# Kernel optimization log

Hardware: AMD Instinct MI355X
Metric: run time of the kernel (lower is better)

## Reference

```python
import jax, jax.numpy as jnp
import numpy as np

EPS = 1e-5  # torch BatchNorm2d default eps

# BinaryActivation with STE: grad zeroed where |x| >= 1 (the extra 1.3 clip in
# xnor_binarize.backward is a subset and thus redundant).
@jax.custom_vjp
def sign_act(x):
    return jnp.sign(x)

def _sa_fwd(x):
    return jnp.sign(x), x

def _sa_bwd(x, g):
    mask = ((x > -1.0) & (x < 1.0)).astype(g.dtype)
    return (g * mask,)

sign_act.defvjp(_sa_fwd, _sa_bwd)

# Weight binarization (scale=False path): w.data.clamp_(-1,1) then sign();
# backward is straight-through identity (|bi_weight|=1 < 1.3 so clip never fires).
@jax.custom_vjp
def bin_weight(w):
    return jnp.sign(jnp.clip(w, -1.0, 1.0))

def _bw_fwd(w):
    return jnp.sign(jnp.clip(w, -1.0, 1.0)), None

def _bw_bwd(_, g):
    return (g,)

bin_weight.defvjp(_bw_fwd, _bw_bwd)


def _branch(x, gamma, beta, w, bias):
    # BatchNorm2d (training-mode batch stats, biased var), affine
    mu = jnp.mean(x, axis=(0, 2, 3), keepdims=True)
    var = jnp.var(x, axis=(0, 2, 3), keepdims=True)
    h = (x - mu) * jax.lax.rsqrt(var + EPS)
    h = h * gamma[None, :, None, None] + beta[None, :, None, None]
    # XNOR conv: binarized activations and weights, stride 2, pad 1
    a = sign_act(h)
    bw = bin_weight(w)
    y = jax.lax.conv_general_dilated(
        a, bw, window_strides=(2, 2), padding=[(1, 1), (1, 1)],
        dimension_numbers=('NCHW', 'OIHW', 'NCHW'))
    y = y + bias[None, :, None, None]
    # shortcut: AvgPool2d(kernel_size=2) (stride defaults to 2)
    B, C, H, W = x.shape
    sc = x.reshape(B, C, H // 2, 2, W // 2, 2).mean(axis=(3, 5))
    return jax.nn.relu(y) + sc


def setup_inputs() -> dict:
    key = jax.random.key(0)
    ks = jax.random.split(key, 9)
    B, C, H, W = 32, 192, 64, 64
    K = 3
    x = jax.random.normal(ks[0], (B, C, H, W), dtype=jnp.float32)
    g1 = 1.0 + 0.1 * jax.random.normal(ks[1], (C,), dtype=jnp.float32)
    b1 = 0.1 * jax.random.normal(ks[2], (C,), dtype=jnp.float32)
    w1 = 0.05 * jax.random.normal(ks[3], (C, C, K, K), dtype=jnp.float32)
    bias1 = jnp.zeros((C,), dtype=jnp.float32)
    g2 = 1.0 + 0.1 * jax.random.normal(ks[4], (C,), dtype=jnp.float32)
    b2 = 0.1 * jax.random.normal(ks[5], (C,), dtype=jnp.float32)
    w2 = 0.05 * jax.random.normal(ks[6], (C, C, K, K), dtype=jnp.float32)
    bias2 = jnp.zeros((C,), dtype=jnp.float32)
    return {"x": x, "g1": g1, "b1": b1, "w1": w1, "bias1": bias1,
            "g2": g2, "b2": b2, "w2": w2, "bias2": bias2}


def reference(x, g1, b1, w1, bias1, g2, b2, w2, bias2):
    x1 = _branch(x, g1, b1, w1, bias1)
    x2 = _branch(x, g2, b2, w2, bias2)
    return jnp.concatenate([x1, x2], axis=1)  # [B, 2C, H/2, W/2]
```

## Files before the change

### kernel.cpp

```cpp
#include <hip/hip_runtime.h>
#include <hip/hip_bf16.h>

typedef unsigned int u32;

#define BN 32
#define CC 192
#define HH 64
#define WW 64
#define HWSZ (HH*WW)
#define OHH 32
#define OWW 32
#define NVALID_SCALE 131072.0f
#define PLW 65
#define PLSZ (PLW*PLW)
#define NPLANE (12*BN)

__global__ __launch_bounds__(256) void k_stats(const float* __restrict__ x,
                                               float* __restrict__ partial) {
    int b = blockIdx.x;
    int c = b >> 5, n = b & 31;
    const float4* p = (const float4*)(x + ((size_t)(n * CC + c) << 12));
    int tid = threadIdx.x;
    float s = 0.f, s2 = 0.f;
#pragma unroll
    for (int k = 0; k < 4; ++k) {
        float4 f = p[tid + 256 * k];
        s  += f.x + f.y + f.z + f.w;
        s2 += f.x * f.x + f.y * f.y + f.z * f.z + f.w * f.w;
    }
#pragma unroll
    for (int off = 32; off > 0; off >>= 1) {
        s  += __shfl_down(s, off, 64);
        s2 += __shfl_down(s2, off, 64);
    }
    __shared__ float red[8];
    int wv = tid >> 6, ln = tid & 63;
    if (ln == 0) { red[wv * 2] = s; red[wv * 2 + 1] = s2; }
    __syncthreads();
    if (tid == 0) {
        partial[b * 2]     = red[0] + red[2] + red[4] + red[6];
        partial[b * 2 + 1] = red[1] + red[3] + red[5] + red[7];
    }
}

__global__ __launch_bounds__(64) void k_coef(const float* __restrict__ partial,
        const float* __restrict__ g1, const float* __restrict__ b1,
        const float* __restrict__ g2, const float* __restrict__ b2,
        float* __restrict__ coef) {
    int c = blockIdx.x;
    int t = threadIdx.x;
    int half = t >> 5, i = t & 31;
    float v = partial[(c * 32 + i) * 2 + half];
#pragma unroll
    for (int off = 16; off > 0; off >>= 1) v += __shfl_down(v, off, 32);
    float S2 = __shfl(v, 32, 64);
    if (t == 0) {
        float S = v;
        const float inv = 1.0f / NVALID_SCALE;
        float mu  = S * inv;
        float var = S2 * inv - mu * mu;
        float r   = 1.0f / sqrtf(var + 1e-5f);
        float s1 = g1[c] * r, t1 = b1[c] - mu * s1;
        float s2 = g2[c] * r, t2 = b2[c] - mu * s2;
        ((float4*)coef)[c] = make_float4(s1, t1, s2, t2);
    }
}

__global__ __launch_bounds__(256) void k_pack_w(const float* __restrict__ w1,
        const float* __restrict__ w2, u32* __restrict__ wp, u32* __restrict__ wsum) {
    __shared__ float wl[CC * 9];
    __shared__ u32 ww[54];
    int b  = blockIdx.x;
    int br = b / CC, oc = b - br * CC;
    const float* W = (br ? w2 : w1) + (size_t)oc * CC * 9;
    int tid = threadIdx.x;
    for (int i = tid; i < CC * 9; i += 256) wl[i] = W[i];
    __syncthreads();
    if (tid < 54) {
        int w6 = tid % 6, pos = tid / 6;
        u32 word = 0;
#pragma unroll
        for (int bb = 0; bb < 32; ++bb) {
            if (wl[(w6 * 32 + bb) * 9 + pos] > 0.f) word |= (1u << bb);
        }
        wp[(size_t)b * 54 + tid] = word;
        ww[tid] = word;
    }
    __syncthreads();
    if (tid == 0) {
        int Wt[9];
#pragma unroll
        for (int t = 0; t < 9; ++t) {
            int s = 0;
#pragma unroll
            for (int w6 = 0; w6 < 6; ++w6) s += __popc(ww[t * 6 + w6]);
            Wt[t] = s;
        }
        wsum[b * 4 + 0] = (u32)(Wt[0] + Wt[1] + Wt[2]);
        wsum[b * 4 + 1] = (u32)(Wt[0] + Wt[3] + Wt[6]);
        wsum[b * 4 + 2] = (u32)Wt[0];
        wsum[b * 4 + 3] = 0;
    }
}

__global__ __launch_bounds__(192) void k_halo(u32* __restrict__ act) {
    u32* pl = act + (size_t)blockIdx.x * PLSZ;
    int t = threadIdx.x;
    if (t < PLW) pl[t] = 0;
    else if (t < 2 * PLW - 1) pl[(t - PLW + 1) * PLW] = 0;
}

__global__ __launch_bounds__(256) void k_pack_act(const float* __restrict__ x,
        const float* __restrict__ coef, u32* __restrict__ act) {
    int tile = blockIdx.x;
    int g    = blockIdx.y;
    int n = tile >> 4, pxt = tile & 15;
    int px = pxt * 256 + threadIdx.x;
    int h = px >> 6, w = px & 63;
    const float*  xb = x + (size_t)n * CC * HWSZ + px;
    const float4* c4 = (const float4*)coef;
    u32 pk1 = 0, pk2 = 0;
#pragma unroll 8
    for (int bb = 0; bb < 32; ++bb) {
        int ch = g * 32 + bb;
        float v = xb[(size_t)ch * HWSZ];
        float4 cf = c4[ch];
        u32 bit = 1u << bb;
        if (v * cf.x + cf.y > 0.f) pk1 |= bit;
        if (v * cf.z + cf.w > 0.f) pk2 |= bit;
    }
    size_t off = (size_t)(h + 1) * PLW + (w + 1);
    act[((size_t)(0 * 6 + g) * BN + n) * PLSZ + off] = pk1;
    act[((size_t)(1 * 6 + g) * BN + n) * PLSZ + off] = pk2;
}

__global__ __launch_bounds__(256, 4) void k_conv(
        const u32* __restrict__ act, const u32* __restrict__ wp,
        const u32* __restrict__ wsum, const float* __restrict__ x,
        const float* __restrict__ bias1, const float* __restrict__ bias2,
        float* __restrict__ out) {
    __shared__ u32 s_act[12 * 5 * PLW];
    int b    = blockIdx.x;
    int tile = b >> 2;
    int n    = tile >> 4, ohp = tile & 15;
    int tid  = threadIdx.x;
    {
        int rowbase = 4 * ohp;
        for (int i = tid; i < 12 * 5 * PLW; i += 256) {
            int q   = i / (5 * PLW);
            int rem = i - q * (5 * PLW);
            s_act[i] = act[((size_t)q * BN + n) * PLSZ + (size_t)rowbase * PLW + rem];
        }
    }
    __syncthreads();
    int wid  = __builtin_amdgcn_readfirstlane((int)(tid >> 6));
    int ocbase = ((b & 3) * 4 + wid) * 12;
    int lane = tid & 63;
    int ow = lane & 31, lh = lane >> 5;
    int oh = 2 * ohp + lh;
    int topE  = (oh == 0), leftE = (ow == 0);
    int nv192 = CC * ((topE ? 2 : 3) * (leftE ? 2 : 3));
    int lloc = (2 * lh) * PLW + 2 * ow;
    float sc[12];
#pragma unroll 1
    for (int br = 0; br < 2; ++br) {
        u32 a[54];
#pragma unroll
        for (int w6 = 0; w6 < 6; ++w6) {
            const u32* ap = &s_act[(br * 6 + w6) * 5 * PLW + lloc];
#pragma unroll
            for (int t = 0; t < 9; ++t) {
                a[t * 6 + w6] = ap[(t / 3) * PLW + (t % 3)];
            }
        }
        const u32*   wqb = wp   + (size_t)(br * CC + ocbase) * 54;
        const u32*   wsb = wsum + (size_t)(br * CC + ocbase) * 4;
        const float* bsp = (br ? bias2 : bias1) + ocbase;
#pragma unroll 2
        for (int j = 0; j < 12; ++j) {
            u32 wv[54];
#pragma unroll
            for (int k = 0; k < 54; ++k) wv[k] = wqb[j * 54 + k];
            int p = 0;
#pragma unroll
            for (int k = 0; k < 54; ++k) p += __popc(a[k] ^ wv[k]);
            int Wr = (int)wsb[j * 4], Wc = (int)wsb[j * 4 + 1], Wk = (int)wsb[j * 4 + 2];
            int corr = (topE ? Wr : 0) + (leftE ? Wc : 0) - ((topE & leftE) ? Wk : 0);
            int dot = nv192 - 2 * p + 2 * corr;
            int oc = ocbase + j;
            float y = (float)dot + bsp[j];
            if (br == 0) {
                const float* xp = x + (((size_t)n * CC + oc) * HH + 2 * oh) * WW + 2 * ow;
                float2 r0 = *(const float2*)xp;
                float2 r1 = *(const float2*)(xp + WW);
                sc[j] = (r0.x + r0.y + r1.x + r1.y) * 0.25f;
            }
            out[((size_t)(n * 384 + br * CC + oc) * OHH + oh) * OWW + ow] =
                fmaxf(y, 0.f) + sc[j];
        }
    }
}

extern "C" void kernel_launch(void* const* d_in, const int* in_sizes, int n_in,
                              void* d_out, int out_size, void* d_ws, size_t ws_size,
                              hipStream_t stream) {
    const float* x     = (const float*)d_in[0];
    const float* g1    = (const float*)d_in[1];
    const float* b1    = (const float*)d_in[2];
    const float* w1    = (const float*)d_in[3];
    const float* bias1 = (const float*)d_in[4];
    const float* g2    = (const float*)d_in[5];
    const float* b2    = (const float*)d_in[6];
    const float* w2    = (const float*)d_in[7];
    const float* bias2 = (const float*)d_in[8];
    float* out = (float*)d_out;
    char* ws = (char*)d_ws;
    float* partial = (float*)(ws);
    float* coef    = (float*)(ws + 49152);
    u32*   wp      = (u32*)  (ws + 52224);
    u32*   wsum    = (u32*)  (ws + 135168);
    u32*   act     = (u32*)  (ws + 141312);

    hipLaunchKernelGGL(k_stats,    dim3(CC * BN),      dim3(256), 0, stream, x, partial);
    hipLaunchKernelGGL(k_coef,     dim3(CC),           dim3(64),  0, stream, partial, g1, b1, g2, b2, coef);
    hipLaunchKernelGGL(k_pack_w,   dim3(2 * CC),       dim3(256), 0, stream, w1, w2, wp, wsum);
    hipLaunchKernelGGL(k_halo,     dim3(NPLANE),       dim3(192), 0, stream, act);
    hipLaunchKernelGGL(k_pack_act, dim3(512, 6),       dim3(256), 0, stream, x, coef, act);
    hipLaunchKernelGGL(k_conv,     dim3(BN * 16 * 4),  dim3(256), 0, stream, act, wp, wsum, x, bias1, bias2, out);
}
```

Before: 248.2 us.

## Deinterleave packed activations by column parity and transpose weight packing for conv

The activation pack kernel now reads float4 per thread and writes each packed row with even and odd columns split into separate halves. Stride-2 conv lanes then read consecutive LDS words, which should cut bank conflicts. Packed weights are laid out so the 12 output channels of a wave are contiguous per (tap, word). The conv loop becomes tap-outer with 12 accumulators instead of holding 54 activation and 54 weight words in registers. This lowers register pressure and makes weight loads uniform across lanes, but it relies on the halo and odd-column offsets (1 and 33) lining up with the padded 65-wide plane.

```diff
diff --git a/kernel.cpp b/kernel.cpp
--- a/kernel.cpp
+++ b/kernel.cpp
@@ -67,11 +67,12 @@
 }
 
 __global__ __launch_bounds__(256) void k_pack_w(const float* __restrict__ w1,
-        const float* __restrict__ w2, u32* __restrict__ wp, u32* __restrict__ wsum) {
+        const float* __restrict__ w2, u32* __restrict__ wp2, u32* __restrict__ wsum) {
     __shared__ float wl[CC * 9];
     __shared__ u32 ww[54];
     int b  = blockIdx.x;
     int br = b / CC, oc = b - br * CC;
+    int g  = oc / 12, j = oc - g * 12;
     const float* W = (br ? w2 : w1) + (size_t)oc * CC * 9;
     int tid = threadIdx.x;
     for (int i = tid; i < CC * 9; i += 256) wl[i] = W[i];
@@ -83,7 +84,7 @@
         for (int bb = 0; bb < 32; ++bb) {
             if (wl[(w6 * 32 + bb) * 9 + pos] > 0.f) word |= (1u << bb);
         }
-        wp[(size_t)b * 54 + tid] = word;
+        wp2[((size_t)(br * 16 + g) * 54 + tid) * 12 + j] = word;
         ww[tid] = word;
     }
     __syncthreads();
@@ -112,30 +113,40 @@
 
 __global__ __launch_bounds__(256) void k_pack_act(const float* __restrict__ x,
         const float* __restrict__ coef, u32* __restrict__ act) {
-    int tile = blockIdx.x;
-    int g    = blockIdx.y;
-    int n = tile >> 4, pxt = tile & 15;
-    int px = pxt * 256 + threadIdx.x;
-    int h = px >> 6, w = px & 63;
-    const float*  xb = x + (size_t)n * CC * HWSZ + px;
+    int bx = blockIdx.x;
+    int g  = blockIdx.y;
+    int n = bx >> 2;
+    int px0 = (bx & 3) * 1024 + threadIdx.x * 4;
+    int h = px0 >> 6, w0 = px0 & 63;
+    const float*  xb = x + (size_t)n * CC * HWSZ + px0;
     const float4* c4 = (const float4*)coef;
-    u32 pk1 = 0, pk2 = 0;
+    u32 p1[4] = {0,0,0,0}, p2[4] = {0,0,0,0};
 #pragma unroll 8
     for (int bb = 0; bb < 32; ++bb) {
         int ch = g * 32 + bb;
-        float v = xb[(size_t)ch * HWSZ];
+        float4 v = *(const float4*)(xb + (size_t)ch * HWSZ);
         float4 cf = c4[ch];
         u32 bit = 1u << bb;
-        if (v * cf.x + cf.y > 0.f) pk1 |= bit;
-        if (v * cf.z + cf.w > 0.f) pk2 |= bit;
-    }
-    size_t off = (size_t)(h + 1) * PLW + (w + 1);
-    act[((size_t)(0 * 6 + g) * BN + n) * PLSZ + off] = pk1;
-    act[((size_t)(1 * 6 + g) * BN + n) * PLSZ + off] = pk2;
+        if (v.x * cf.x + cf.y > 0.f) p1[0] |= bit;
+        if (v.y * cf.x + cf.y > 0.f) p1[1] |= bit;
+        if (v.z * cf.x + cf.y > 0.f) p1[2] |= bit;
+        if (v.w * cf.x + cf.y > 0.f) p1[3] |= bit;
+        if (v.x * cf.z + cf.w > 0.f) p2[0] |= bit;
+        if (v.y * cf.z + cf.w > 0.f) p2[1] |= bit;
+        if (v.z * cf.z + cf.w > 0.f) p2[2] |= bit;
+        if (v.w * cf.z + cf.w > 0.f) p2[3] |= bit;
+    }
+    size_t rb1 = ((size_t)(0 * 6 + g) * BN + n) * PLSZ + (size_t)(h + 1) * PLW;
+    size_t rb2 = ((size_t)(1 * 6 + g) * BN + n) * PLSZ + (size_t)(h + 1) * PLW;
+    int ei = w0 / 2 + 1, oi = 33 + w0 / 2;
+    *(uint2*)(act + rb1 + ei) = make_uint2(p1[1], p1[3]);
+    *(uint2*)(act + rb1 + oi) = make_uint2(p1[0], p1[2]);
+    *(uint2*)(act + rb2 + ei) = make_uint2(p2[1], p2[3]);
+    *(uint2*)(act + rb2 + oi) = make_uint2(p2[0], p2[2]);
 }
 
 __global__ __launch_bounds__(256, 4) void k_conv(
-        const u32* __restrict__ act, const u32* __restrict__ wp,
+        const u32* __restrict__ act, const u32* __restrict__ wp2,
         const u32* __restrict__ wsum, const float* __restrict__ x,
         const float* __restrict__ bias1, const float* __restrict__ bias2,
         float* __restrict__ out) {
@@ -154,39 +165,40 @@
     }
     __syncthreads();
     int wid  = __builtin_amdgcn_readfirstlane((int)(tid >> 6));
-    int ocbase = ((b & 3) * 4 + wid) * 12;
+    int g    = (b & 3) * 4 + wid;
+    int ocbase = g * 12;
     int lane = tid & 63;
     int ow = lane & 31, lh = lane >> 5;
     int oh = 2 * ohp + lh;
     int topE  = (oh == 0), leftE = (ow == 0);
     int nv192 = CC * ((topE ? 2 : 3) * (leftE ? 2 : 3));
-    int lloc = (2 * lh) * PLW + 2 * ow;
     float sc[12];
 #pragma unroll 1
     for (int br = 0; br < 2; ++br) {
-        u32 a[54];
-#pragma unroll
-        for (int w6 = 0; w6 < 6; ++w6) {
-            const u32* ap = &s_act[(br * 6 + w6) * 5 * PLW + lloc];
-#pragma unroll
-            for (int t = 0; t < 9; ++t) {
-                a[t * 6 + w6] = ap[(t / 3) * PLW + (t % 3)];
+        const u32* ap  = &s_act[br * (6 * 5 * PLW) + (2 * lh) * PLW + ow];
+        const u32* wq2 = wp2 + (size_t)(br * 16 + g) * 648;
+        int acc[12];
+#pragma unroll
+        for (int j = 0; j < 12; ++j) acc[j] = 0;
+#pragma unroll
+        for (int t = 0; t < 9; ++t) {
+            int kh = t / 3, kw = t % 3;
+            int coff = (kw == 0) ? 0 : (kw == 1 ? 33 : 1);
+#pragma unroll
+            for (int w6 = 0; w6 < 6; ++w6) {
+                u32 av = ap[w6 * (5 * PLW) + kh * PLW + coff];
+                const u32* wr = wq2 + (t * 6 + w6) * 12;
+#pragma unroll
+                for (int j = 0; j < 12; ++j) acc[j] += __popc(av ^ wr[j]);
             }
         }
-        const u32*   wqb = wp   + (size_t)(br * CC + ocbase) * 54;
         const u32*   wsb = wsum + (size_t)(br * CC + ocbase) * 4;
         const float* bsp = (br ? bias2 : bias1) + ocbase;
-#pragma unroll 2
+#pragma unroll
         for (int j = 0; j < 12; ++j) {
-            u32 wv[54];
-#pragma unroll
-            for (int k = 0; k < 54; ++k) wv[k] = wqb[j * 54 + k];
-            int p = 0;
-#pragma unroll
-            for (int k = 0; k < 54; ++k) p += __popc(a[k] ^ wv[k]);
             int Wr = (int)wsb[j * 4], Wc = (int)wsb[j * 4 + 1], Wk = (int)wsb[j * 4 + 2];
             int corr = (topE ? Wr : 0) + (leftE ? Wc : 0) - ((topE & leftE) ? Wk : 0);
-            int dot = nv192 - 2 * p + 2 * corr;
+            int dot = nv192 - 2 * acc[j] + 2 * corr;
             int oc = ocbase + j;
             float y = (float)dot + bsp[j];
             if (br == 0) {
@@ -217,14 +229,14 @@
     char* ws = (char*)d_ws;
     float* partial = (float*)(ws);
     float* coef    = (float*)(ws + 49152);
-    u32*   wp      = (u32*)  (ws + 52224);
+    u32*   wp2     = (u32*)  (ws + 52224);
     u32*   wsum    = (u32*)  (ws + 135168);
     u32*   act     = (u32*)  (ws + 141312);
 
     hipLaunchKernelGGL(k_stats,    dim3(CC * BN),      dim3(256), 0, stream, x, partial);
     hipLaunchKernelGGL(k_coef,     dim3(CC),           dim3(64),  0, stream, partial, g1, b1, g2, b2, coef);
-    hipLaunchKernelGGL(k_pack_w,   dim3(2 * CC),       dim3(256), 0, stream, w1, w2, wp, wsum);
+    hipLaunchKernelGGL(k_pack_w,   dim3(2 * CC),       dim3(256), 0, stream, w1, w2, wp2, wsum);
     hipLaunchKernelGGL(k_halo,     dim3(NPLANE),       dim3(192), 0, stream, act);
-    hipLaunchKernelGGL(k_pack_act, dim3(512, 6),       dim3(256), 0, stream, x, coef, act);
-    hipLaunchKernelGGL(k_conv,     dim3(BN * 16 * 4),  dim3(256), 0, stream, act, wp, wsum, x, bias1, bias2, out);
-}
+    hipLaunchKernelGGL(k_pack_act, dim3(128, 6),       dim3(256), 0, stream, x, coef, act);
+    hipLaunchKernelGGL(k_conv,     dim3(BN * 16 * 4),  dim3(256), 0, stream, act, wp2, wsum, x, bias1, bias2, out);
+}
```

Measured after the change: 479.0 us. 1.93x slower.
